# Kernel tuning notes

Measured on AMD Instinct MI355X. Metric: run time of the kernel, lower is better.

Reference implementation:

```python
import jax, jax.numpy as jnp
import numpy as np

N_TOKENS = 2048
HIDDEN = 2048
N_EXPERTS = 8
TOP_K = 2
D_FF = 1408  # per-expert SwiGLU intermediate size


def setup_inputs() -> dict:
    key = jax.random.key(0)
    k_h, k_g, k_wg, k_wu, k_wd = jax.random.split(key, 5)
    s_in = 1.0 / np.sqrt(HIDDEN)
    s_ff = 1.0 / np.sqrt(D_FF)
    return {
        "h": jax.random.normal(k_h, (N_TOKENS, HIDDEN), dtype=jnp.float32),
        "gate_w": jax.random.normal(k_g, (N_EXPERTS, HIDDEN), dtype=jnp.float32) * s_in,
        "w_gate": jax.random.normal(k_wg, (N_EXPERTS, HIDDEN, D_FF), dtype=jnp.float32) * s_in,
        "w_up": jax.random.normal(k_wu, (N_EXPERTS, HIDDEN, D_FF), dtype=jnp.float32) * s_in,
        "w_down": jax.random.normal(k_wd, (N_EXPERTS, D_FF, HIDDEN), dtype=jnp.float32) * s_ff,
    }


def reference(h, gate_w, w_gate, w_up, w_down):
    # --- gate: linear (fp32) + softmax + top-k (no renorm, as in source) ---
    logits = jnp.einsum("nd,ed->ne", h.astype(jnp.float32), gate_w.astype(jnp.float32))
    scores = jax.nn.softmax(logits, axis=-1)                 # [N, E]
    topk_weight, topk_idx = jax.lax.top_k(scores, TOP_K)     # [N, K], [N, K]

    # --- per-expert SwiGLU MLP applied densely, then gather selected experts ---
    # (same math as the per-expert grouped GEMM dispatch in the eager loop)
    g = jnp.einsum("nd,edf->enf", h, w_gate)                 # [E, N, F]
    u = jnp.einsum("nd,edf->enf", h, w_up)                   # [E, N, F]
    y = jnp.einsum("enf,efd->end", jax.nn.silu(g) * u, w_down)  # [E, N, D]

    # gather each token's top-k expert outputs: [N, K, D]
    y_tok = jnp.transpose(y, (1, 0, 2))                      # [N, E, D]
    sel = jnp.take_along_axis(y_tok, topk_idx[:, :, None], axis=1)

    # weighted combine
    out = jnp.einsum("nk,nkd->nd", topk_weight.astype(h.dtype), sel)
    return out
```

## Files before the change

kernel.cpp:

```cpp
#include <hip/hip_runtime.h>
#include <hip/hip_bf16.h>
#include <stdint.h>

#define N_TOK 2048
#define HID   2048
#define NEXP  8
#define DFF   1408

typedef __attribute__((ext_vector_type(8))) short short8;
typedef __attribute__((ext_vector_type(4))) float f32x4;

__device__ __forceinline__ unsigned short f2bf(float f) {
  union { float ff; uint32_t u; } v; v.ff = f;
  return (unsigned short)((v.u + 0x7FFFu + ((v.u >> 16) & 1u)) >> 16);
}
__device__ __forceinline__ float bf2f(unsigned short u) {
  union { uint32_t i; float f; } v; v.i = (uint32_t)u << 16; return v.f;
}

__device__ __forceinline__ void gl2lds16(const void* g, void* l) {
  __builtin_amdgcn_global_load_lds(
      (const __attribute__((address_space(1))) void*)g,
      (__attribute__((address_space(3))) void*)l, 16, 0, 0);
}

#define MFMA16(a, b, c) __builtin_amdgcn_mfma_f32_16x16x32_bf16((a), (b), (c), 0, 0, 0)

__global__ __launch_bounds__(256) void gate_topk_k(
    const float* __restrict__ h, const float* __restrict__ gw,
    int* __restrict__ cnt, int* __restrict__ topk_idx, float* __restrict__ topk_w,
    unsigned short* __restrict__ hbf)
{
  int token = blockIdx.x * 4 + (threadIdx.x >> 6);
  int lane  = threadIdx.x & 63;
  const float* hr = h + (size_t)token * HID;
  float acc[NEXP];
#pragma unroll
  for (int e = 0; e < NEXP; ++e) acc[e] = 0.f;
  for (int c = lane * 8; c < HID; c += 512) {
    float4 a = *(const float4*)(hr + c);
    float4 b = *(const float4*)(hr + c + 4);
    unsigned short o[8] = {f2bf(a.x), f2bf(a.y), f2bf(a.z), f2bf(a.w),
                           f2bf(b.x), f2bf(b.y), f2bf(b.z), f2bf(b.w)};
    *(short8*)&hbf[(size_t)token * HID + c] = *(const short8*)o;
#pragma unroll
    for (int e = 0; e < NEXP; ++e) {
      const float* gp = gw + (size_t)e * HID + c;
      float4 ga = *(const float4*)gp;
      float4 gb = *(const float4*)(gp + 4);
      acc[e] = fmaf(a.x, ga.x, fmaf(a.y, ga.y, fmaf(a.z, ga.z, fmaf(a.w, ga.w,
               fmaf(b.x, gb.x, fmaf(b.y, gb.y, fmaf(b.z, gb.z, fmaf(b.w, gb.w, acc[e]))))))));
    }
  }
#pragma unroll
  for (int e = 0; e < NEXP; ++e) {
    float a = acc[e];
#pragma unroll
    for (int s = 32; s > 0; s >>= 1) a += __shfl_xor(a, s, 64);
    acc[e] = a;
  }
  if (lane == 0) {
    float m = acc[0];
#pragma unroll
    for (int e = 1; e < NEXP; ++e) m = fmaxf(m, acc[e]);
    float w[NEXP]; float s = 0.f;
#pragma unroll
    for (int e = 0; e < NEXP; ++e) { w[e] = __expf(acc[e] - m); s += w[e]; }
    float inv = 1.f / s;
    int i0 = 0; float b0 = acc[0];
#pragma unroll
    for (int e = 1; e < NEXP; ++e) if (acc[e] > b0) { b0 = acc[e]; i0 = e; }
    int i1 = -1; float b1 = -3.4e38f;
#pragma unroll
    for (int e = 0; e < NEXP; ++e) if (e != i0 && acc[e] > b1) { b1 = acc[e]; i1 = e; }
    topk_idx[token * 2 + 0] = i0;
    topk_idx[token * 2 + 1] = i1;
    topk_w[token * 2 + 0] = w[i0] * inv;
    topk_w[token * 2 + 1] = w[i1] * inv;
    atomicAdd(&cnt[i0], 1);
    atomicAdd(&cnt[i1], 1);
  }
}

__global__ void prefix_k(const int* __restrict__ cnt, int* __restrict__ offs,
                         int* __restrict__ cursor) {
  if (threadIdx.x == 0 && blockIdx.x == 0) {
    int s = 0;
    for (int e = 0; e < NEXP; ++e) { offs[e] = s; cursor[e] = s; s += cnt[e]; }
  }
}

__global__ __launch_bounds__(256) void scatter_k(
    const int* __restrict__ topk_idx, const float* __restrict__ topk_w,
    int* __restrict__ cursor, int* __restrict__ pair_token, float* __restrict__ pair_w,
    int* __restrict__ tok_slot)
{
  int n = blockIdx.x * 256 + threadIdx.x;
  if (n >= N_TOK) return;
#pragma unroll
  for (int k = 0; k < 2; ++k) {
    int e = topk_idx[n * 2 + k];
    int p = atomicAdd(&cursor[e], 1);
    pair_token[p] = n;
    pair_w[p] = topk_w[n * 2 + k];
    tok_slot[n * 2 + k] = p;
  }
}

__global__ __launch_bounds__(256) void transpose_k(const float* __restrict__ s1,
                                                   unsigned short* __restrict__ d1,
                                                   const float* __restrict__ s2,
                                                   unsigned short* __restrict__ d2,
                                                   int R, int C, int nz1)
{
  __shared__ unsigned short T[64 * 66];
  const size_t sl = (size_t)R * C;
  int z = blockIdx.z;
  const float* s; unsigned short* d;
  if (z < nz1) { s = s1 + (size_t)z * sl; d = d1 + (size_t)z * sl; }
  else { s = s2 + (size_t)(z - nz1) * sl; d = d2 + (size_t)(z - nz1) * sl; }
  const int rb = blockIdx.x * 64, cb = blockIdx.y * 64;
  const int t = threadIdx.x;
  const int tr = t >> 4, tc = (t & 15) * 4;
  const float* sp = s + (size_t)(rb + tr) * C + cb + tc;
#pragma unroll
  for (int i = 0; i < 4; ++i) {
    float4 v = *(const float4*)(sp + (size_t)i * 16 * C);
    int r = tr + i * 16;
    uint32_t p0 = (uint32_t)f2bf(v.x) | ((uint32_t)f2bf(v.y) << 16);
    uint32_t p1 = (uint32_t)f2bf(v.z) | ((uint32_t)f2bf(v.w) << 16);
    *(uint32_t*)&T[r * 66 + tc]     = p0;
    *(uint32_t*)&T[r * 66 + tc + 2] = p1;
  }
  __syncthreads();
  const int f = t >> 2, ch = (t & 3) * 16;
  unsigned short* dp = d + (size_t)(cb + f) * R + rb + ch;
#pragma unroll
  for (int g = 0; g < 2; ++g) {
    unsigned short buf[8];
#pragma unroll
    for (int j = 0; j < 8; ++j) buf[j] = T[(ch + g * 8 + j) * 66 + f];
    *(short8*)(dp + g * 8) = *(const short8*)buf;
  }
}

__global__ __launch_bounds__(256) void gateup12_k(
    const unsigned short* __restrict__ hbf,
    const unsigned short* __restrict__ wgt, const unsigned short* __restrict__ wut,
    const int* __restrict__ cnt, const int* __restrict__ offs,
    const int* __restrict__ pair_token, unsigned short* __restrict__ act,
    int e_fixed, int nw, int nbcnt, size_t wstride)
{
  const int x = blockIdx.x;
  const int wti = x % nw;
  int e, nb;
  if (e_fixed >= 0) { e = e_fixed; nb = wti; }
  else { e = wti / nbcnt; nb = wti % nbcnt; }
  const int count = cnt[e];
  const int off = offs[e];
  const int c0 = nb * 64;

  __shared__ unsigned short As[128 * 32];
  __shared__ unsigned short Bg[64 * 32];
  __shared__ unsigned short Bu[64 * 32];
  __shared__ int tok[128];

  const int t = threadIdx.x;
  const int w = t >> 6, l = t & 63;
  const int lr = l >> 2;
  const int lp = l & 3;
  const int sc = (lp ^ (lr & 3)) * 8;

  const size_t wb = (e_fixed >= 0) ? 0 : (size_t)e * wstride;
  const unsigned short* gP = wgt + wb + (size_t)(c0 + w * 16 + lr) * HID + sc;
  const unsigned short* uP = wut + wb + (size_t)(c0 + w * 16 + lr) * HID + sc;

  const int fr = l & 15, fq = l >> 4;
  const int wr = (w >> 1) * 64, wc = (w & 1) * 32;

  for (int mb = x / nw; mb * 128 < count; mb += 8) {
    const int m0 = mb * 128;
    const int rows = min(128, count - m0);
    if (t < 128) tok[t] = pair_token[off + m0 + min(t, rows - 1)];
    __syncthreads();

    const unsigned short* aP0 = hbf + (size_t)tok[w * 32 + lr] * HID + sc;
    const unsigned short* aP1 = hbf + (size_t)tok[w * 32 + 16 + lr] * HID + sc;

    f32x4 accg[4][2], accu[4][2];
#pragma unroll
    for (int i = 0; i < 4; ++i)
#pragma unroll
      for (int j = 0; j < 2; ++j) {
        accg[i][j] = (f32x4){0.f, 0.f, 0.f, 0.f};
        accu[i][j] = (f32x4){0.f, 0.f, 0.f, 0.f};
      }

    for (int kt = 0; kt < HID; kt += 32) {
      gl2lds16(aP0 + kt, &As[(w * 32) * 32]);
      gl2lds16(aP1 + kt, &As[(w * 32 + 16) * 32]);
      gl2lds16(gP + kt, &Bg[(w * 16) * 32]);
      gl2lds16(uP + kt, &Bu[(w * 16) * 32]);
      __syncthreads();

      short8 af[4], bg[2], bu[2];
#pragma unroll
      for (int mi = 0; mi < 4; ++mi) {
        int r = wr + mi * 16 + fr;
        af[mi] = *(const short8*)&As[r * 32 + ((fq ^ (r & 3)) * 8)];
      }
#pragma unroll
      for (int ni = 0; ni < 2; ++ni) {
        int rb = wc + ni * 16 + fr;
        bg[ni] = *(const short8*)&Bg[rb * 32 + ((fq ^ (rb & 3)) * 8)];
        bu[ni] = *(const short8*)&Bu[rb * 32 + ((fq ^ (rb & 3)) * 8)];
      }
#pragma unroll
      for (int mi = 0; mi < 4; ++mi)
#pragma unroll
        for (int ni = 0; ni < 2; ++ni) {
          accg[mi][ni] = MFMA16(af[mi], bg[ni], accg[mi][ni]);
          accu[mi][ni] = MFMA16(af[mi], bu[ni], accu[mi][ni]);
        }
      __syncthreads();
    }

#pragma unroll
    for (int mi = 0; mi < 4; ++mi)
#pragma unroll
      for (int ni = 0; ni < 2; ++ni)
#pragma unroll
        for (int j = 0; j < 4; ++j) {
          int r = wr + mi * 16 + fq * 4 + j;
          if (r < rows) {
            float g = accg[mi][ni][j], u = accu[mi][ni][j];
            float a = (g / (1.f + __expf(-g))) * u;
            act[(size_t)(off + m0 + r) * DFF + (c0 + wc + ni * 16 + fr)] = f2bf(a);
          }
        }
  }
}

__global__ __launch_bounds__(256) void down12_k(
    const unsigned short* __restrict__ act, const unsigned short* __restrict__ wdt,
    const int* __restrict__ cnt, const int* __restrict__ offs,
    unsigned short* __restrict__ ypair, int e_fixed, int nw, int nbcnt, size_t wstride)
{
  const int x = blockIdx.x;
  const int wti = x % nw;
  int e, nb;
  if (e_fixed >= 0) { e = e_fixed; nb = wti; }
  else { e = wti / nbcnt; nb = wti % nbcnt; }
  const int count = cnt[e];
  const int off = offs[e];
  const int c0 = nb * 128;

  __shared__ unsigned short As[128 * 32];
  __shared__ unsigned short Bd[128 * 32];

  const int t = threadIdx.x;
  const int w = t >> 6, l = t & 63;
  const int lr = l >> 2;
  const int lp = l & 3;
  const int sc = (lp ^ (lr & 3)) * 8;

  const size_t wb = (e_fixed >= 0) ? 0 : (size_t)e * wstride;
  const unsigned short* bP0 = wdt + wb + (size_t)(c0 + w * 32 + lr) * DFF + sc;
  const unsigned short* bP1 = wdt + wb + (size_t)(c0 + w * 32 + 16 + lr) * DFF + sc;

  const int fr = l & 15, fq = l >> 4;
  const int wr = (w >> 1) * 64, wc = (w & 1) * 64;

  for (int mb = x / nw; mb * 128 < count; mb += 8) {
    const int m0 = mb * 128;
    const int rows = min(128, count - m0);
    const int ra0 = min(w * 32 + lr, rows - 1);
    const int ra1 = min(w * 32 + 16 + lr, rows - 1);
    const unsigned short* aP0 = act + (size_t)(off + m0 + ra0) * DFF + sc;
    const unsigned short* aP1 = act + (size_t)(off + m0 + ra1) * DFF + sc;

    f32x4 acc[4][4];
#pragma unroll
    for (int i = 0; i < 4; ++i)
#pragma unroll
      for (int j = 0; j < 4; ++j) acc[i][j] = (f32x4){0.f, 0.f, 0.f, 0.f};

    for (int kt = 0; kt < DFF; kt += 32) {
      gl2lds16(aP0 + kt, &As[(w * 32) * 32]);
      gl2lds16(aP1 + kt, &As[(w * 32 + 16) * 32]);
      gl2lds16(bP0 + kt, &Bd[(w * 32) * 32]);
      gl2lds16(bP1 + kt, &Bd[(w * 32 + 16) * 32]);
      __syncthreads();

      short8 af[4], bd[4];
#pragma unroll
      for (int mi = 0; mi < 4; ++mi) {
        int r = wr + mi * 16 + fr;
        af[mi] = *(const short8*)&As[r * 32 + ((fq ^ (r & 3)) * 8)];
      }
#pragma unroll
      for (int ni = 0; ni < 4; ++ni) {
        int rb = wc + ni * 16 + fr;
        bd[ni] = *(const short8*)&Bd[rb * 32 + ((fq ^ (rb & 3)) * 8)];
      }
#pragma unroll
      for (int mi = 0; mi < 4; ++mi)
#pragma unroll
        for (int ni = 0; ni < 4; ++ni)
          acc[mi][ni] = MFMA16(af[mi], bd[ni], acc[mi][ni]);
      __syncthreads();
    }

#pragma unroll
    for (int mi = 0; mi < 4; ++mi)
#pragma unroll
      for (int ni = 0; ni < 4; ++ni)
#pragma unroll
        for (int j = 0; j < 4; ++j) {
          int r = wr + mi * 16 + fq * 4 + j;
          if (r < rows)
            ypair[(size_t)(off + m0 + r) * HID + (c0 + wc + ni * 16 + fr)] = f2bf(acc[mi][ni][j]);
        }
  }
}

__global__ __launch_bounds__(256) void combine_k(
    const unsigned short* __restrict__ ypair, const int* __restrict__ tok_slot,
    const float* __restrict__ topk_w, float* __restrict__ out)
{
  int i = blockIdx.x * 256 + threadIdx.x;
  int n = i >> 8;
  int dv = (i & 255) * 8;
  int s0 = tok_slot[n * 2], s1 = tok_slot[n * 2 + 1];
  float w0 = topk_w[n * 2], w1 = topk_w[n * 2 + 1];
  short8 a = *(const short8*)&ypair[(size_t)s0 * HID + dv];
  short8 b = *(const short8*)&ypair[(size_t)s1 * HID + dv];
  float o[8];
#pragma unroll
  for (int j = 0; j < 8; ++j)
    o[j] = w0 * bf2f((unsigned short)a[j]) + w1 * bf2f((unsigned short)b[j]);
  *(float4*)&out[(size_t)n * HID + dv]     = *(const float4*)&o[0];
  *(float4*)&out[(size_t)n * HID + dv + 4] = *(const float4*)&o[4];
}

extern "C" void kernel_launch(void* const* d_in, const int* in_sizes, int n_in,
                              void* d_out, int out_size, void* d_ws, size_t ws_size,
                              hipStream_t stream) {
  const float* h  = (const float*)d_in[0];
  const float* gw = (const float*)d_in[1];
  const float* wg = (const float*)d_in[2];
  const float* wu = (const float*)d_in[3];
  const float* wd = (const float*)d_in[4];
  float* out = (float*)d_out;

  const size_t SL = (size_t)DFF * HID;
  char* ws = (char*)d_ws;
  int*   cnt        = (int*)(ws + 0);
  int*   offs       = (int*)(ws + 32);
  int*   cursor     = (int*)(ws + 64);
  int*   pair_token = (int*)(ws + 256);
  float* pair_w     = (float*)(ws + 16640);
  int*   tok_slot   = (int*)(ws + 33024);
  int*   topk_idx   = (int*)(ws + 49408);
  float* topk_w     = (float*)(ws + 65792);
  unsigned short* act = (unsigned short*)(ws + 82176);
  unsigned short* hbf = (unsigned short*)(ws + 11616512);
  unsigned short* wgt = (unsigned short*)(ws + 20005120);
  unsigned short* wut = (unsigned short*)(ws + 66142464);
  unsigned short* ypair_full = (unsigned short*)(ws + 66142464);
  const size_t NEED_FULL = 112279808ull;

  hipMemsetAsync(ws, 0, 256, stream);

  gate_topk_k<<<N_TOK / 4, 256, 0, stream>>>(h, gw, cnt, topk_idx, topk_w, hbf);
  prefix_k<<<1, 64, 0, stream>>>(cnt, offs, cursor);
  scatter_k<<<N_TOK / 256, 256, 0, stream>>>(topk_idx, topk_w, cursor, pair_token, pair_w, tok_slot);

  if (ws_size >= NEED_FULL) {
    transpose_k<<<dim3(HID / 64, DFF / 64, 16), 256, 0, stream>>>(wg, wgt, wu, wut, HID, DFF, 8);
    gateup12_k<<<176 * 8, 256, 0, stream>>>(hbf, wgt, wut, cnt, offs, pair_token, act,
                                            -1, 176, 22, SL);
    transpose_k<<<dim3(DFF / 64, HID / 64, 8), 256, 0, stream>>>(wd, wgt, wd, wgt, DFF, HID, 8);
    down12_k<<<128 * 8, 256, 0, stream>>>(act, wgt, cnt, offs, ypair_full,
                                          -1, 128, 16, SL);
    combine_k<<<(N_TOK * HID / 8) / 256, 256, 0, stream>>>(ypair_full, tok_slot, topk_w, out);
  } else {
    unsigned short* wgtE = (unsigned short*)(ws + 20005120);
    unsigned short* wutE = (unsigned short*)(ws + 25772288);
    unsigned short* ypair = (unsigned short*)(ws + 31539456);
    for (int e = 0; e < NEXP; ++e) {
      transpose_k<<<dim3(HID / 64, DFF / 64, 2), 256, 0, stream>>>(wg + e * SL, wgtE, wu + e * SL, wutE, HID, DFF, 1);
      gateup12_k<<<22 * 8, 256, 0, stream>>>(hbf, wgtE, wutE, cnt, offs, pair_token, act,
                                             e, 22, 22, 0);
    }
    for (int e = 0; e < NEXP; ++e) {
      transpose_k<<<dim3(DFF / 64, HID / 64, 1), 256, 0, stream>>>(wd + e * SL, wgtE, wd + e * SL, wgtE, DFF, HID, 1);
      down12_k<<<16 * 8, 256, 0, stream>>>(act, wgtE, cnt, offs, ypair, e, 16, 16, 0);
    }
    combine_k<<<(N_TOK * HID / 8) / 256, 256, 0, stream>>>(ypair, tok_slot, topk_w, out);
  }
}
```

Baseline: 332.7 us.

## Use 512-row M tiles with double-buffered LDS pipelining in expert GEMMs

Both expert GEMM kernels now give each block one 512-row chunk of an expert's tokens instead of looping over 128-row tiles. The gate/up kernel moves to 512 threads, with half the waves loading gate weights and half loading up weights. The down kernel narrows its N tile to 64 columns. Both kernels double-buffer LDS with explicit vmcnt waits and raw barriers, use a new swizzle, and raise wave priority around the MFMA sequence. The aim is fewer reloads of weight tiles and overlap of global-to-LDS loads with MFMA work. The cost is larger LDS use, higher register pressure, and wasted work on partial 512-row chunks when expert counts are just over a chunk boundary.

```diff
diff --git a/kernel.cpp b/kernel.cpp
--- a/kernel.cpp
+++ b/kernel.cpp
@@ -144,7 +144,7 @@
   }
 }
 
-__global__ __launch_bounds__(256) void gateup12_k(
+__global__ __launch_bounds__(512) void gateup14_k(
     const unsigned short* __restrict__ hbf,
     const unsigned short* __restrict__ wgt, const unsigned short* __restrict__ wut,
     const int* __restrict__ cnt, const int* __restrict__ offs,
@@ -152,176 +152,204 @@
     int e_fixed, int nw, int nbcnt, size_t wstride)
 {
   const int x = blockIdx.x;
-  const int wti = x % nw;
+  const int wti = x % nw, mc = x / nw;
   int e, nb;
   if (e_fixed >= 0) { e = e_fixed; nb = wti; }
   else { e = wti / nbcnt; nb = wti % nbcnt; }
   const int count = cnt[e];
+  if (mc * 512 >= count) return;
   const int off = offs[e];
+  const int m0 = mc * 512;
+  const int rows = min(512, count - m0);
   const int c0 = nb * 64;
 
-  __shared__ unsigned short As[128 * 32];
-  __shared__ unsigned short Bg[64 * 32];
-  __shared__ unsigned short Bu[64 * 32];
-  __shared__ int tok[128];
+  __shared__ unsigned short As[2][512 * 32];
+  __shared__ unsigned short Bg[2][64 * 32];
+  __shared__ unsigned short Bu[2][64 * 32];
+  __shared__ int tok[512];
 
   const int t = threadIdx.x;
+  tok[t] = pair_token[off + m0 + min(t, rows - 1)];
+  __syncthreads();
+
   const int w = t >> 6, l = t & 63;
-  const int lr = l >> 2;
-  const int lp = l & 3;
-  const int sc = (lp ^ (lr & 3)) * 8;
+  const int lr = l >> 2, lp = l & 3;
+  const int swz = (lp ^ ((lr >> 1) & 3)) * 8;
 
   const size_t wb = (e_fixed >= 0) ? 0 : (size_t)e * wstride;
-  const unsigned short* gP = wgt + wb + (size_t)(c0 + w * 16 + lr) * HID + sc;
-  const unsigned short* uP = wut + wb + (size_t)(c0 + w * 16 + lr) * HID + sc;
+  const unsigned short* aP[4];
+#pragma unroll
+  for (int i = 0; i < 4; ++i)
+    aP[i] = hbf + (size_t)tok[w * 64 + i * 16 + lr] * HID + swz;
+  const unsigned short* bsrc = (w < 4)
+      ? wgt + wb + (size_t)(c0 + w * 16 + lr) * HID + swz
+      : wut + wb + (size_t)(c0 + (w - 4) * 16 + lr) * HID + swz;
+  const int ldsA = (w * 64) * 32;
+  const int ldsB = ((w & 3) * 16) * 32;
 
   const int fr = l & 15, fq = l >> 4;
-  const int wr = (w >> 1) * 64, wc = (w & 1) * 32;
-
-  for (int mb = x / nw; mb * 128 < count; mb += 8) {
-    const int m0 = mb * 128;
-    const int rows = min(128, count - m0);
-    if (t < 128) tok[t] = pair_token[off + m0 + min(t, rows - 1)];
-    __syncthreads();
-
-    const unsigned short* aP0 = hbf + (size_t)tok[w * 32 + lr] * HID + sc;
-    const unsigned short* aP1 = hbf + (size_t)tok[w * 32 + 16 + lr] * HID + sc;
-
-    f32x4 accg[4][2], accu[4][2];
+  const int rch = (fq ^ ((fr >> 1) & 3)) * 8;
+
+  f32x4 accg[4][4], accu[4][4];
+#pragma unroll
+  for (int i = 0; i < 4; ++i)
+#pragma unroll
+    for (int j = 0; j < 4; ++j) {
+      accg[i][j] = (f32x4){0.f, 0.f, 0.f, 0.f};
+      accu[i][j] = (f32x4){0.f, 0.f, 0.f, 0.f};
+    }
+
+  auto stage = [&](int b, int kt) {
 #pragma unroll
     for (int i = 0; i < 4; ++i)
-#pragma unroll
-      for (int j = 0; j < 2; ++j) {
-        accg[i][j] = (f32x4){0.f, 0.f, 0.f, 0.f};
-        accu[i][j] = (f32x4){0.f, 0.f, 0.f, 0.f};
+      gl2lds16(aP[i] + kt, &As[b][ldsA + i * 16 * 32]);
+    if (w < 4) gl2lds16(bsrc + kt, &Bg[b][ldsB]);
+    else       gl2lds16(bsrc + kt, &Bu[b][ldsB]);
+  };
+  auto compute = [&](int b) {
+    short8 af[4], bg[4], bu[4];
+#pragma unroll
+    for (int mi = 0; mi < 4; ++mi)
+      af[mi] = *(const short8*)&As[b][(w * 64 + mi * 16 + fr) * 32 + rch];
+#pragma unroll
+    for (int ni = 0; ni < 4; ++ni) {
+      bg[ni] = *(const short8*)&Bg[b][(ni * 16 + fr) * 32 + rch];
+      bu[ni] = *(const short8*)&Bu[b][(ni * 16 + fr) * 32 + rch];
+    }
+    __builtin_amdgcn_s_setprio(1);
+#pragma unroll
+    for (int mi = 0; mi < 4; ++mi)
+#pragma unroll
+      for (int ni = 0; ni < 4; ++ni) {
+        accg[mi][ni] = MFMA16(af[mi], bg[ni], accg[mi][ni]);
+        accu[mi][ni] = MFMA16(af[mi], bu[ni], accu[mi][ni]);
       }
-
-    for (int kt = 0; kt < HID; kt += 32) {
-      gl2lds16(aP0 + kt, &As[(w * 32) * 32]);
-      gl2lds16(aP1 + kt, &As[(w * 32 + 16) * 32]);
-      gl2lds16(gP + kt, &Bg[(w * 16) * 32]);
-      gl2lds16(uP + kt, &Bu[(w * 16) * 32]);
-      __syncthreads();
-
-      short8 af[4], bg[2], bu[2];
-#pragma unroll
-      for (int mi = 0; mi < 4; ++mi) {
-        int r = wr + mi * 16 + fr;
-        af[mi] = *(const short8*)&As[r * 32 + ((fq ^ (r & 3)) * 8)];
+    __builtin_amdgcn_s_setprio(0);
+  };
+
+  const int NK = HID / 32;
+  stage(0, 0);
+  int cur = 0;
+  for (int k = 0; k + 1 < NK; ++k) {
+    stage(cur ^ 1, (k + 1) * 32);
+    asm volatile("s_waitcnt vmcnt(5)" ::: "memory");
+    asm volatile("s_barrier" ::: "memory");
+    compute(cur);
+    asm volatile("s_barrier" ::: "memory");
+    cur ^= 1;
+  }
+  asm volatile("s_waitcnt vmcnt(0)" ::: "memory");
+  asm volatile("s_barrier" ::: "memory");
+  compute(cur);
+
+#pragma unroll
+  for (int mi = 0; mi < 4; ++mi)
+#pragma unroll
+    for (int ni = 0; ni < 4; ++ni)
+#pragma unroll
+      for (int j = 0; j < 4; ++j) {
+        int r = w * 64 + mi * 16 + fq * 4 + j;
+        if (r < rows) {
+          float g = accg[mi][ni][j], u = accu[mi][ni][j];
+          float a = (g / (1.f + __expf(-g))) * u;
+          act[(size_t)(off + m0 + r) * DFF + (c0 + ni * 16 + fr)] = f2bf(a);
+        }
       }
-#pragma unroll
-      for (int ni = 0; ni < 2; ++ni) {
-        int rb = wc + ni * 16 + fr;
-        bg[ni] = *(const short8*)&Bg[rb * 32 + ((fq ^ (rb & 3)) * 8)];
-        bu[ni] = *(const short8*)&Bu[rb * 32 + ((fq ^ (rb & 3)) * 8)];
-      }
-#pragma unroll
-      for (int mi = 0; mi < 4; ++mi)
-#pragma unroll
-        for (int ni = 0; ni < 2; ++ni) {
-          accg[mi][ni] = MFMA16(af[mi], bg[ni], accg[mi][ni]);
-          accu[mi][ni] = MFMA16(af[mi], bu[ni], accu[mi][ni]);
-        }
-      __syncthreads();
-    }
-
-#pragma unroll
-    for (int mi = 0; mi < 4; ++mi)
-#pragma unroll
-      for (int ni = 0; ni < 2; ++ni)
-#pragma unroll
-        for (int j = 0; j < 4; ++j) {
-          int r = wr + mi * 16 + fq * 4 + j;
-          if (r < rows) {
-            float g = accg[mi][ni][j], u = accu[mi][ni][j];
-            float a = (g / (1.f + __expf(-g))) * u;
-            act[(size_t)(off + m0 + r) * DFF + (c0 + wc + ni * 16 + fr)] = f2bf(a);
-          }
-        }
-  }
-}
-
-__global__ __launch_bounds__(256) void down12_k(
+}
+
+__global__ __launch_bounds__(256) void down14_k(
     const unsigned short* __restrict__ act, const unsigned short* __restrict__ wdt,
     const int* __restrict__ cnt, const int* __restrict__ offs,
     unsigned short* __restrict__ ypair, int e_fixed, int nw, int nbcnt, size_t wstride)
 {
   const int x = blockIdx.x;
-  const int wti = x % nw;
-  int e, nb;
-  if (e_fixed >= 0) { e = e_fixed; nb = wti; }
-  else { e = wti / nbcnt; nb = wti % nbcnt; }
+  const int wti = x % nw, mc = x / nw;
+  int e, nc;
+  if (e_fixed >= 0) { e = e_fixed; nc = wti; }
+  else { e = wti / nbcnt; nc = wti % nbcnt; }
   const int count = cnt[e];
+  if (mc * 512 >= count) return;
   const int off = offs[e];
-  const int c0 = nb * 128;
-
-  __shared__ unsigned short As[128 * 32];
-  __shared__ unsigned short Bd[128 * 32];
+  const int m0 = mc * 512;
+  const int rows = min(512, count - m0);
+  const int c0 = nc * 64;
+
+  __shared__ unsigned short As[2][512 * 32];
+  __shared__ unsigned short Bd[2][64 * 32];
 
   const int t = threadIdx.x;
   const int w = t >> 6, l = t & 63;
-  const int lr = l >> 2;
-  const int lp = l & 3;
-  const int sc = (lp ^ (lr & 3)) * 8;
+  const int lr = l >> 2, lp = l & 3;
+  const int swz = (lp ^ ((lr >> 1) & 3)) * 8;
 
   const size_t wb = (e_fixed >= 0) ? 0 : (size_t)e * wstride;
-  const unsigned short* bP0 = wdt + wb + (size_t)(c0 + w * 32 + lr) * DFF + sc;
-  const unsigned short* bP1 = wdt + wb + (size_t)(c0 + w * 32 + 16 + lr) * DFF + sc;
+  const unsigned short* aP[8];
+#pragma unroll
+  for (int i = 0; i < 8; ++i) {
+    int r = min(w * 128 + i * 16 + lr, rows - 1);
+    aP[i] = act + (size_t)(off + m0 + r) * DFF + swz;
+  }
+  const unsigned short* bsrc = wdt + wb + (size_t)(c0 + w * 16 + lr) * DFF + swz;
+  const int ldsA = (w * 128) * 32;
+  const int ldsB = (w * 16) * 32;
 
   const int fr = l & 15, fq = l >> 4;
-  const int wr = (w >> 1) * 64, wc = (w & 1) * 64;
-
-  for (int mb = x / nw; mb * 128 < count; mb += 8) {
-    const int m0 = mb * 128;
-    const int rows = min(128, count - m0);
-    const int ra0 = min(w * 32 + lr, rows - 1);
-    const int ra1 = min(w * 32 + 16 + lr, rows - 1);
-    const unsigned short* aP0 = act + (size_t)(off + m0 + ra0) * DFF + sc;
-    const unsigned short* aP1 = act + (size_t)(off + m0 + ra1) * DFF + sc;
-
-    f32x4 acc[4][4];
-#pragma unroll
-    for (int i = 0; i < 4; ++i)
-#pragma unroll
-      for (int j = 0; j < 4; ++j) acc[i][j] = (f32x4){0.f, 0.f, 0.f, 0.f};
-
-    for (int kt = 0; kt < DFF; kt += 32) {
-      gl2lds16(aP0 + kt, &As[(w * 32) * 32]);
-      gl2lds16(aP1 + kt, &As[(w * 32 + 16) * 32]);
-      gl2lds16(bP0 + kt, &Bd[(w * 32) * 32]);
-      gl2lds16(bP1 + kt, &Bd[(w * 32 + 16) * 32]);
-      __syncthreads();
-
-      short8 af[4], bd[4];
-#pragma unroll
-      for (int mi = 0; mi < 4; ++mi) {
-        int r = wr + mi * 16 + fr;
-        af[mi] = *(const short8*)&As[r * 32 + ((fq ^ (r & 3)) * 8)];
+  const int rch = (fq ^ ((fr >> 1) & 3)) * 8;
+
+  f32x4 acc[8][4];
+#pragma unroll
+  for (int i = 0; i < 8; ++i)
+#pragma unroll
+    for (int j = 0; j < 4; ++j) acc[i][j] = (f32x4){0.f, 0.f, 0.f, 0.f};
+
+  auto stage = [&](int b, int kt) {
+#pragma unroll
+    for (int i = 0; i < 8; ++i)
+      gl2lds16(aP[i] + kt, &As[b][ldsA + i * 16 * 32]);
+    gl2lds16(bsrc + kt, &Bd[b][ldsB]);
+  };
+  auto compute = [&](int b) {
+    short8 af[8], bd[4];
+#pragma unroll
+    for (int mi = 0; mi < 8; ++mi)
+      af[mi] = *(const short8*)&As[b][(w * 128 + mi * 16 + fr) * 32 + rch];
+#pragma unroll
+    for (int ni = 0; ni < 4; ++ni)
+      bd[ni] = *(const short8*)&Bd[b][(ni * 16 + fr) * 32 + rch];
+    __builtin_amdgcn_s_setprio(1);
+#pragma unroll
+    for (int mi = 0; mi < 8; ++mi)
+#pragma unroll
+      for (int ni = 0; ni < 4; ++ni)
+        acc[mi][ni] = MFMA16(af[mi], bd[ni], acc[mi][ni]);
+    __builtin_amdgcn_s_setprio(0);
+  };
+
+  const int NK = DFF / 32;
+  stage(0, 0);
+  int cur = 0;
+  for (int k = 0; k + 1 < NK; ++k) {
+    stage(cur ^ 1, (k + 1) * 32);
+    asm volatile("s_waitcnt vmcnt(9)" ::: "memory");
+    asm volatile("s_barrier" ::: "memory");
+    compute(cur);
+    asm volatile("s_barrier" ::: "memory");
+    cur ^= 1;
+  }
+  asm volatile("s_waitcnt vmcnt(0)" ::: "memory");
+  asm volatile("s_barrier" ::: "memory");
+  compute(cur);
+
+#pragma unroll
+  for (int mi = 0; mi < 8; ++mi)
+#pragma unroll
+    for (int ni = 0; ni < 4; ++ni)
+#pragma unroll
+      for (int j = 0; j < 4; ++j) {
+        int r = w * 128 + mi * 16 + fq * 4 + j;
+        if (r < rows)
+          ypair[(size_t)(off + m0 + r) * HID + (c0 + ni * 16 + fr)] = f2bf(acc[mi][ni][j]);
       }
-#pragma unroll
-      for (int ni = 0; ni < 4; ++ni) {
-        int rb = wc + ni * 16 + fr;
-        bd[ni] = *(const short8*)&Bd[rb * 32 + ((fq ^ (rb & 3)) * 8)];
-      }
-#pragma unroll
-      for (int mi = 0; mi < 4; ++mi)
-#pragma unroll
-        for (int ni = 0; ni < 4; ++ni)
-          acc[mi][ni] = MFMA16(af[mi], bd[ni], acc[mi][ni]);
-      __syncthreads();
-    }
-
-#pragma unroll
-    for (int mi = 0; mi < 4; ++mi)
-#pragma unroll
-      for (int ni = 0; ni < 4; ++ni)
-#pragma unroll
-        for (int j = 0; j < 4; ++j) {
-          int r = wr + mi * 16 + fq * 4 + j;
-          if (r < rows)
-            ypair[(size_t)(off + m0 + r) * HID + (c0 + wc + ni * 16 + fr)] = f2bf(acc[mi][ni][j]);
-        }
-  }
 }
 
 __global__ __launch_bounds__(256) void combine_k(
@@ -378,11 +406,11 @@
 
   if (ws_size >= NEED_FULL) {
     transpose_k<<<dim3(HID / 64, DFF / 64, 16), 256, 0, stream>>>(wg, wgt, wu, wut, HID, DFF, 8);
-    gateup12_k<<<176 * 8, 256, 0, stream>>>(hbf, wgt, wut, cnt, offs, pair_token, act,
+    gateup14_k<<<176 * 4, 512, 0, stream>>>(hbf, wgt, wut, cnt, offs, pair_token, act,
                                             -1, 176, 22, SL);
     transpose_k<<<dim3(DFF / 64, HID / 64, 8), 256, 0, stream>>>(wd, wgt, wd, wgt, DFF, HID, 8);
-    down12_k<<<128 * 8, 256, 0, stream>>>(act, wgt, cnt, offs, ypair_full,
-                                          -1, 128, 16, SL);
+    down14_k<<<256 * 4, 256, 0, stream>>>(act, wgt, cnt, offs, ypair_full,
+                                          -1, 256, 32, SL);
     combine_k<<<(N_TOK * HID / 8) / 256, 256, 0, stream>>>(ypair_full, tok_slot, topk_w, out);
   } else {
     unsigned short* wgtE = (unsigned short*)(ws + 20005120);
@@ -390,12 +418,12 @@
     unsigned short* ypair = (unsigned short*)(ws + 31539456);
     for (int e = 0; e < NEXP; ++e) {
       transpose_k<<<dim3(HID / 64, DFF / 64, 2), 256, 0, stream>>>(wg + e * SL, wgtE, wu + e * SL, wutE, HID, DFF, 1);
-      gateup12_k<<<22 * 8, 256, 0, stream>>>(hbf, wgtE, wutE, cnt, offs, pair_token, act,
+      gateup14_k<<<22 * 4, 512, 0, stream>>>(hbf, wgtE, wutE, cnt, offs, pair_token, act,
                                              e, 22, 22, 0);
     }
     for (int e = 0; e < NEXP; ++e) {
       transpose_k<<<dim3(DFF / 64, HID / 64, 1), 256, 0, stream>>>(wd + e * SL, wgtE, wd + e * SL, wgtE, DFF, HID, 1);
-      down12_k<<<16 * 8, 256, 0, stream>>>(act, wgtE, cnt, offs, ypair, e, 16, 16, 0);
+      down14_k<<<32 * 4, 256, 0, stream>>>(act, wgtE, cnt, offs, ypair, e, 32, 32, 0);
     }
     combine_k<<<(N_TOK * HID / 8) / 256, 256, 0, stream>>>(ypair, tok_slot, topk_w, out);
   }
```

After: 398.2 us. 1.2x slower.
